# Optimization experiments

Measured on AMD Instinct MI355X. Metric: run time of the kernel, lower is better.

Reference implementation:

```python
import jax, jax.numpy as jnp
import numpy as np

NUM_HEADS = 16
QMAX = 127.0  # int8 symmetric

def fake_quant(x):
    # symmetric per-tensor int8 quantize -> dequantize (models Quantize/QLinear numerics)
    scale = jnp.maximum(jnp.max(jnp.abs(x)) / QMAX, 1e-8)
    q = jnp.clip(jnp.round(x / scale), -QMAX, QMAX) * scale
    # straight-through estimator (no-op in fwd-only, keeps fwd/bwd code identical)
    return x + jax.lax.stop_gradient(q - x)

def setup_inputs() -> dict:
    key = jax.random.key(0)
    ks = jax.random.split(key, 5)
    B, T, C = 2, 2048, 1024
    return {
        "x": jax.random.normal(ks[0], (B, T, C), jnp.float32),
        "Wqkv": jax.random.normal(ks[1], (3 * C, C), jnp.float32) * (C ** -0.5),
        "bqkv": jax.random.normal(ks[2], (3 * C,), jnp.float32) * 0.01,
        "Wproj": jax.random.normal(ks[3], (C, C), jnp.float32) * (C ** -0.5),
        "bproj": jax.random.normal(ks[4], (C,), jnp.float32) * 0.01,
    }

def reference(x, Wqkv, bqkv, Wproj, bproj):
    B, T, C = x.shape
    H = NUM_HEADS
    D = C // H
    scale = D ** -0.5
    # quantized input + quantized-weight linear (dequantized to fp32 afterwards)
    xq = fake_quant(x)
    qkv = xq @ fake_quant(Wqkv).T + bqkv                      # [B, T, 3C]
    qkv = qkv.reshape(B, T, 3, H, D).transpose(2, 0, 3, 1, 4)  # [3, B, H, T, D]
    q, k, v = qkv[0], qkv[1], qkv[2]
    scores = jnp.einsum("bhqd,bhkd->bhqk", q, k) * scale       # [B, H, T, T]
    causal = jnp.triu(jnp.full((T, T), -jnp.inf, jnp.float32), k=1)
    attn = jax.nn.softmax(scores + causal, axis=-1)
    # dropout: eval mode -> identity
    out = jnp.einsum("bhqk,bhkd->bhqd", attn, v)               # [B, H, T, D]
    out = out.transpose(0, 2, 1, 3).reshape(B, T, C)
    outq = fake_quant(out)
    return outq @ fake_quant(Wproj).T + bproj
```

## Files before the change

### kernel.cpp

```cpp
#include <hip/hip_runtime.h>
#include <hip/hip_bf16.h>
#include <stdint.h>

typedef __bf16 bf16_t;
typedef bf16_t bf16x4 __attribute__((ext_vector_type(4)));
typedef bf16_t bf16x8 __attribute__((ext_vector_type(8)));
typedef short s16x4 __attribute__((ext_vector_type(4)));
typedef int i32x4 __attribute__((ext_vector_type(4)));
typedef float f32x4 __attribute__((ext_vector_type(4)));

#define QMAXF 127.0f

__device__ __forceinline__ void gl16(const void* g, void* l) {
  __builtin_amdgcn_global_load_lds(
      (__attribute__((address_space(1))) void*)(g),
      (__attribute__((address_space(3))) void*)(l), 16, 0, 0);
}

__global__ __launch_bounds__(256) void amax3_kernel(const float* __restrict__ p0, int n0,
                                                    const float* __restrict__ p1, int n1,
                                                    const float* __restrict__ p2, int n2,
                                                    float* __restrict__ dst) {
  const float* p; int n; float* d; int b0, nb;
  if (blockIdx.x < 512)      { p = p0; n = n0; d = dst + 0; b0 = 0;   nb = 512; }
  else if (blockIdx.x < 768) { p = p1; n = n1; d = dst + 1; b0 = 512; nb = 256; }
  else                       { p = p2; n = n2; d = dst + 2; b0 = 768; nb = 128; }
  const int n4 = n >> 2;
  const int stride = nb * 256;
  float m = 0.f;
  for (int i = (blockIdx.x - b0) * 256 + threadIdx.x; i < n4; i += stride) {
    const f32x4 v = ((const f32x4*)p)[i];
    m = fmaxf(m, fmaxf(fmaxf(fabsf(v[0]), fabsf(v[1])), fmaxf(fabsf(v[2]), fabsf(v[3]))));
  }
#pragma unroll
  for (int dd = 1; dd < 64; dd <<= 1) m = fmaxf(m, __shfl_xor(m, dd));
  __shared__ float sm[4];
  if ((threadIdx.x & 63) == 0) sm[threadIdx.x >> 6] = m;
  __syncthreads();
  if (threadIdx.x == 0) {
    float mm = fmaxf(fmaxf(sm[0], sm[1]), fmaxf(sm[2], sm[3]));
    atomicMax((int*)d, __float_as_int(mm));
  }
}

__device__ __forceinline__ void quant_body(const float* __restrict__ p, int n,
                                           const float* __restrict__ amax,
                                           int8_t* __restrict__ q, int bid, int nb) {
  const float s = fmaxf(amax[0] / QMAXF, 1e-8f);
  const int n4 = n >> 2;
  const int stride = nb * 256;
  for (int i = bid * 256 + (int)threadIdx.x; i < n4; i += stride) {
    const f32x4 v = ((const f32x4*)p)[i];
    int r[4];
#pragma unroll
    for (int j = 0; j < 4; j++) {
      float t = rintf(v[j] / s);
      t = fminf(127.f, fmaxf(-127.f, t));
      r[j] = (int)t;
    }
    ((uint32_t*)q)[i] = (uint32_t)(r[0] & 0xff) | ((uint32_t)(r[1] & 0xff) << 8) |
                        ((uint32_t)(r[2] & 0xff) << 16) | ((uint32_t)(r[3] & 0xff) << 24);
  }
}

__global__ __launch_bounds__(256) void quant3_kernel(const float* __restrict__ p0, int n0,
                                                     const float* __restrict__ p1, int n1,
                                                     const float* __restrict__ p2, int n2,
                                                     const float* __restrict__ amax,
                                                     int8_t* __restrict__ q0,
                                                     int8_t* __restrict__ q1,
                                                     int8_t* __restrict__ q2) {
  if (blockIdx.x < 512)      quant_body(p0, n0, amax + 0, q0, blockIdx.x, 512);
  else if (blockIdx.x < 768) quant_body(p1, n1, amax + 1, q1, blockIdx.x - 512, 256);
  else                       quant_body(p2, n2, amax + 2, q2, blockIdx.x - 768, 128);
}

__global__ __launch_bounds__(256) void quant_kernel(const float* __restrict__ p, int n,
                                                    const float* __restrict__ amax,
                                                    int8_t* __restrict__ q) {
  quant_body(p, n, amax, q, blockIdx.x, gridDim.x);
}

template <int MODE>
__global__ __launch_bounds__(256) void gemm_i8_kernel(
    const int8_t* __restrict__ A, const int8_t* __restrict__ Bw,
    const float* __restrict__ amaxA, const float* __restrict__ amaxB,
    const float* __restrict__ bias,
    bf16_t* __restrict__ qkv_out, bf16_t* __restrict__ vt_out, float* __restrict__ f_out) {
  constexpr int K = 1024;
  __shared__ int8_t As[128 * 64];
  __shared__ int8_t Bs[128 * 64];
  const int tid = threadIdx.x;
  const int lane = tid & 63;
  const int w = tid >> 6, wr = w >> 1, wc = w & 1;
  const int l15 = lane & 15, lg = lane >> 4;
  const int bm = blockIdx.y * 128, bn = blockIdx.x * 128;

  const int sr = tid >> 2;
  const int sc = (tid & 3) * 16;
  const int8_t* gA = A + (size_t)(bm + sr) * K + sc;
  const int8_t* gB = Bw + (size_t)(bn + sr) * K + sc;
  int8_t* lA = As + tid * 16;
  int8_t* lB = Bs + tid * 16;

  i32x4 acc[4][4] = {};

  for (int k0 = 0; k0 < K; k0 += 64) {
    __syncthreads();
    gl16(gA + k0, lA);
    gl16(gA + 64 * K + k0, lA + 4096);
    gl16(gB + k0, lB);
    gl16(gB + 64 * K + k0, lB + 4096);
    __syncthreads();
    i32x4 aF[4], bF[4];
#pragma unroll
    for (int m = 0; m < 4; m++)
      aF[m] = *(const i32x4*)(As + (wr * 64 + m * 16 + l15) * 64 + lg * 16);
#pragma unroll
    for (int n = 0; n < 4; n++)
      bF[n] = *(const i32x4*)(Bs + (wc * 64 + n * 16 + l15) * 64 + lg * 16);
#pragma unroll
    for (int m = 0; m < 4; m++)
#pragma unroll
      for (int n = 0; n < 4; n++)
        acc[m][n] = __builtin_amdgcn_mfma_i32_16x16x64_i8(aF[m], bF[n], acc[m][n], 0, 0, 0);
  }

  const float sA = fmaxf(amaxA[0] / QMAXF, 1e-8f);
  const float sB = fmaxf(amaxB[0] / QMAXF, 1e-8f);
  const float s = sA * sB;

#pragma unroll
  for (int m = 0; m < 4; m++) {
#pragma unroll
    for (int n = 0; n < 4; n++) {
      const int c = bn + wc * 64 + n * 16 + l15;
      const float bs = bias[c];
      const int r0 = bm + wr * 64 + m * 16 + lg * 4;
      float vv[4];
#pragma unroll
      for (int reg = 0; reg < 4; reg++) vv[reg] = (float)acc[m][n][reg] * s + bs;
      if (MODE == 0) {
        const int which = c >> 10, hd = c & 1023;
        if (which < 2) {
#pragma unroll
          for (int reg = 0; reg < 4; reg++) {
            const int r = r0 + reg;
            const int b = r >> 11, t = r & 2047;
            qkv_out[(size_t)which * (32u * 2048 * 64) +
                    (size_t)((((b << 4) + (hd >> 6)) * 2048 + t) << 6) + (hd & 63)] = (bf16_t)vv[reg];
          }
        } else {
          const int b = r0 >> 11, t0 = r0 & 2047;
          const int h = hd >> 6, d = hd & 63;
          bf16x4 pk;
#pragma unroll
          for (int reg = 0; reg < 4; reg++) pk[reg] = (bf16_t)vv[reg];
          *(bf16x4*)(vt_out + ((size_t)((b << 4) + h) * 64 + d) * 2048 + t0) = pk;
        }
      } else {
#pragma unroll
        for (int reg = 0; reg < 4; reg++) f_out[(size_t)(r0 + reg) * 1024 + c] = vv[reg];
      }
    }
  }
}

__global__ __launch_bounds__(128) void attn_kernel(
    const bf16_t* __restrict__ Qg, const bf16_t* __restrict__ Kg, const bf16_t* __restrict__ VTg,
    float* __restrict__ Out, float* __restrict__ amax_out) {
  const int bh = blockIdx.x;
  const int pairi = blockIdx.y;
  const int tid = threadIdx.x, lane = tid & 63, w = tid >> 6;
  const int l15 = lane & 15, lg = lane >> 4;
  const int b = bh >> 4, h = bh & 15;

  const bf16_t* Qp = Qg + (size_t)bh * 2048 * 64;
  const char* Kbase = (const char*)(Kg + (size_t)bh * 2048 * 64);
  const char* Vbase = (const char*)(VTg + (size_t)bh * 64 * 2048);

  __shared__ __align__(16) bf16_t Kb[2][4096];
  __shared__ __align__(16) bf16_t Vb[2][4096];

  float am = 0.f;
  const float CSC = 0.18033688f;

  auto stage = [&](int kv0, int buf) {
#pragma unroll
    for (int i = 0; i < 8; i++) {
      const int o = i * 1024 + lane * 16;
      const int row = o >> 7;
      const int sbc = (o & 127) ^ ((row & 7) << 4);
      if (w == 0)
        gl16(Kbase + (size_t)(kv0 + row) * 128 + sbc, (char*)Kb[buf] + o);
      else
        gl16(Vbase + (size_t)row * 4096 + (size_t)kv0 * 2 + sbc, (char*)Vb[buf] + o);
    }
  };

  for (int half = 0; half < 2; ++half) {
    const int S = half ? (63 - pairi) : pairi;
    const int qb = S * 32 + w * 16;
    const int nt = (S >> 1) + 1;
    const int qrow = qb + l15;

    bf16x8 qf[2];
#pragma unroll
    for (int ks = 0; ks < 2; ks++)
      qf[ks] = *(const bf16x8*)(Qp + (size_t)(qb + l15) * 64 + ks * 32 + lg * 8);

    f32x4 acc[4] = {};
    float mrow = -1e30f, lsum = 0.f;

    stage(0, 0);
    __syncthreads();

    for (int it = 0; it < nt; ++it) {
      const int cur = it & 1;
      const int kv0 = it * 64;
      if (it + 1 < nt) stage(kv0 + 64, cur ^ 1);

      bf16x8 kF[4][2];
#pragma unroll
      for (int rf = 0; rf < 4; rf++)
#pragma unroll
        for (int ks = 0; ks < 2; ks++) {
          const int row = rf * 16 + l15;
          kF[rf][ks] = *(const bf16x8*)((const char*)Kb[cur] + row * 128 +
                                        ((ks * 64 + lg * 16) ^ ((row & 7) << 4)));
        }
      f32x4 sfT[4] = {};
      __builtin_amdgcn_s_setprio(1);
#pragma unroll
      for (int rf = 0; rf < 4; rf++)
#pragma unroll
        for (int ks = 0; ks < 2; ks++)
          sfT[rf] = __builtin_amdgcn_mfma_f32_16x16x32_bf16(kF[rf][ks], qf[ks], sfT[rf], 0, 0, 0);
      __builtin_amdgcn_s_setprio(0);

      s16x4 vB[4][4];
#pragma unroll
      for (int cf = 0; cf < 4; cf++)
#pragma unroll
        for (int rf = 0; rf < 4; rf++) {
          const int row = cf * 16 + l15;
          vB[cf][rf] = *(const s16x4*)((const char*)Vb[cur] + row * 128 +
                                       (((rf * 32 + lg * 8)) ^ ((row & 7) << 4)));
        }

      float a[16];
      const bool need_mask = (it == nt - 1);
#pragma unroll
      for (int rf = 0; rf < 4; rf++)
#pragma unroll
        for (int reg = 0; reg < 4; reg++) {
          float v = sfT[rf][reg] * CSC;
          if (need_mask && (kv0 + rf * 16 + lg * 4 + reg > qrow)) v = -1e30f;
          a[rf * 4 + reg] = v;
        }
      float mx = a[0];
#pragma unroll
      for (int i = 1; i < 16; i++) mx = fmaxf(mx, a[i]);
      mx = fmaxf(mx, __shfl_xor(mx, 16));
      mx = fmaxf(mx, __shfl_xor(mx, 32));

      if (!__all(mx <= mrow + 11.5416f)) {
        const float mnew = fmaxf(mrow, mx);
        const float alpha = __builtin_amdgcn_exp2f(mrow - mnew);
        float av[4];
#pragma unroll
        for (int reg = 0; reg < 4; reg++) av[reg] = __shfl(alpha, lg * 4 + reg);
#pragma unroll
        for (int cf = 0; cf < 4; cf++)
#pragma unroll
          for (int reg = 0; reg < 4; reg++) acc[cf][reg] *= av[reg];
        lsum *= alpha;
        mrow = mnew;
      }

      float p[16], rs = 0.f;
#pragma unroll
      for (int i = 0; i < 16; i++) { p[i] = __builtin_amdgcn_exp2f(a[i] - mrow); rs += p[i]; }
      rs += __shfl_xor(rs, 16);
      rs += __shfl_xor(rs, 32);
      lsum += rs;

      s16x4 pa[4];
#pragma unroll
      for (int rf = 0; rf < 4; rf++) {
        bf16x4 t;
#pragma unroll
        for (int reg = 0; reg < 4; reg++) t[reg] = (bf16_t)p[rf * 4 + reg];
        pa[rf] = __builtin_bit_cast(s16x4, t);
      }
      __builtin_amdgcn_s_setprio(1);
#pragma unroll
      for (int cf = 0; cf < 4; cf++)
#pragma unroll
        for (int rf = 0; rf < 4; rf++)
          acc[cf] = __builtin_amdgcn_mfma_f32_16x16x16bf16_1k(pa[rf], vB[cf][rf], acc[cf], 0, 0, 0);
      __builtin_amdgcn_s_setprio(0);

      __syncthreads();
    }

    const float inv = 1.0f / lsum;
    float iq[4];
#pragma unroll
    for (int reg = 0; reg < 4; reg++) iq[reg] = __shfl(inv, lg * 4 + reg);
#pragma unroll
    for (int cf = 0; cf < 4; cf++)
#pragma unroll
      for (int reg = 0; reg < 4; reg++) {
        const float v = acc[cf][reg] * iq[reg];
        am = fmaxf(am, fabsf(v));
        const int t = qb + lg * 4 + reg;
        Out[(size_t)(b * 2048 + t) * 1024 + h * 64 + cf * 16 + l15] = v;
      }
  }

#pragma unroll
  for (int dd = 1; dd < 64; dd <<= 1) am = fmaxf(am, __shfl_xor(am, dd));
  if (lane == 0) atomicMax((int*)amax_out, __float_as_int(am));
}

extern "C" void kernel_launch(void* const* d_in, const int* in_sizes, int n_in,
                              void* d_out, int out_size, void* d_ws, size_t ws_size,
                              hipStream_t stream) {
  const float* x = (const float*)d_in[0];
  const float* Wqkv = (const float*)d_in[1];
  const float* bqkv = (const float*)d_in[2];
  const float* Wproj = (const float*)d_in[3];
  const float* bproj = (const float*)d_in[4];
  float* out = (float*)d_out;

  char* ws = (char*)d_ws;
  float* amax = (float*)ws;
  int8_t* xq = (int8_t*)(ws + 256);
  int8_t* wqq = xq + (size_t)4096 * 1024;
  int8_t* wpq = wqq + (size_t)3072 * 1024;
  bf16_t* qkv = (bf16_t*)(ws + 8388864);
  bf16_t* Q = qkv;
  bf16_t* Kk = qkv + (size_t)32 * 2048 * 64;
  bf16_t* VT = qkv + (size_t)2 * 32 * 2048 * 64;
  float* aout = (float*)(ws + 33554688);
  int8_t* outq = (int8_t*)(ws + 50331904);

  hipMemsetAsync(amax, 0, 16, stream);
  amax3_kernel<<<896, 256, 0, stream>>>(x, 4194304, Wqkv, 3145728, Wproj, 1048576, amax);
  quant3_kernel<<<896, 256, 0, stream>>>(x, 4194304, Wqkv, 3145728, Wproj, 1048576, amax,
                                         xq, wqq, wpq);
  gemm_i8_kernel<0><<<dim3(24, 32), 256, 0, stream>>>(xq, wqq, amax + 0, amax + 1, bqkv,
                                                      qkv, VT, nullptr);
  attn_kernel<<<dim3(32, 32), 128, 0, stream>>>(Q, Kk, VT, aout, amax + 3);
  quant_kernel<<<512, 256, 0, stream>>>(aout, 4194304, amax + 3, outq);
  gemm_i8_kernel<1><<<dim3(8, 32), 256, 0, stream>>>(outq, wpq, amax + 3, amax + 2, bproj,
                                                     nullptr, nullptr, out);
}
```

Baseline: 144.4 us.

## Split attention into one query tile per block, single-buffer V, fold scale into Q

Attention blocks now each handle one 32-row query tile, launched heaviest-first over a 64-wide grid, instead of pairing a light and a heavy tile in one block. V staging becomes single-buffered, with a mid-iteration barrier so the next V tile loads after the current one has been read into registers. This halves V shared memory, which may raise occupancy. The softmax scale constant is multiplied into Q in the QKV GEMM epilogue, removing a per-score multiply. In exchange the kernel launches more blocks, adds a second barrier per iteration, and stores Q with an extra bf16 rounding after the scaling.

```diff
diff --git a/kernel.cpp b/kernel.cpp
--- a/kernel.cpp
+++ b/kernel.cpp
@@ -10,6 +10,7 @@
 typedef float f32x4 __attribute__((ext_vector_type(4)));
 
 #define QMAXF 127.0f
+#define CSC 0.18033688f
 
 __device__ __forceinline__ void gl16(const void* g, void* l) {
   __builtin_amdgcn_global_load_lds(
@@ -143,12 +144,14 @@
       if (MODE == 0) {
         const int which = c >> 10, hd = c & 1023;
         if (which < 2) {
+          const float qs = (which == 0) ? CSC : 1.0f;
 #pragma unroll
           for (int reg = 0; reg < 4; reg++) {
             const int r = r0 + reg;
             const int b = r >> 11, t = r & 2047;
             qkv_out[(size_t)which * (32u * 2048 * 64) +
-                    (size_t)((((b << 4) + (hd >> 6)) * 2048 + t) << 6) + (hd & 63)] = (bf16_t)vv[reg];
+                    (size_t)((((b << 4) + (hd >> 6)) * 2048 + t) << 6) + (hd & 63)] =
+                (bf16_t)(vv[reg] * qs);
           }
         } else {
           const int b = r0 >> 11, t0 = r0 & 2047;
@@ -170,7 +173,7 @@
     const bf16_t* __restrict__ Qg, const bf16_t* __restrict__ Kg, const bf16_t* __restrict__ VTg,
     float* __restrict__ Out, float* __restrict__ amax_out) {
   const int bh = blockIdx.x;
-  const int pairi = blockIdx.y;
+  const int S = 63 - (int)blockIdx.y;
   const int tid = threadIdx.x, lane = tid & 63, w = tid >> 6;
   const int l15 = lane & 15, lg = lane >> 4;
   const int b = bh >> 4, h = bh & 15;
@@ -180,144 +183,157 @@
   const char* Vbase = (const char*)(VTg + (size_t)bh * 64 * 2048);
 
   __shared__ __align__(16) bf16_t Kb[2][4096];
-  __shared__ __align__(16) bf16_t Vb[2][4096];
-
+  __shared__ __align__(16) bf16_t Vb[4096];
+
+  auto stageK = [&](int kv0, int buf) {
+    if (w == 0) {
+#pragma unroll
+      for (int i = 0; i < 8; i++) {
+        const int o = i * 1024 + lane * 16;
+        const int row = o >> 7;
+        const int sbc = (o & 127) ^ ((row & 7) << 4);
+        gl16(Kbase + (size_t)(kv0 + row) * 128 + sbc, (char*)Kb[buf] + o);
+      }
+    }
+  };
+  auto stageV = [&](int kv0) {
+    if (w == 1) {
+#pragma unroll
+      for (int i = 0; i < 8; i++) {
+        const int o = i * 1024 + lane * 16;
+        const int row = o >> 7;
+        const int sbc = (o & 127) ^ ((row & 7) << 4);
+        gl16(Vbase + (size_t)row * 4096 + (size_t)kv0 * 2 + sbc, (char*)Vb + o);
+      }
+    }
+  };
+
+  const int qb = S * 32 + w * 16;
+  const int nt = (S >> 1) + 1;
+  const int qrow = qb + l15;
+
+  bf16x8 qf[2];
+#pragma unroll
+  for (int ks = 0; ks < 2; ks++)
+    qf[ks] = *(const bf16x8*)(Qp + (size_t)(qb + l15) * 64 + ks * 32 + lg * 8);
+
+  f32x4 acc[4] = {};
+  float mrow = -1e30f, lsum = 0.f;
+
+  stageK(0, 0);
+  stageV(0);
+  __syncthreads();
+
+  for (int it = 0; it < nt; ++it) {
+    const int cur = it & 1;
+    const int kv0 = it * 64;
+    if (it + 1 < nt) stageK(kv0 + 64, cur ^ 1);
+
+    bf16x8 kF[4][2];
+#pragma unroll
+    for (int rf = 0; rf < 4; rf++)
+#pragma unroll
+      for (int ks = 0; ks < 2; ks++) {
+        const int row = rf * 16 + l15;
+        kF[rf][ks] = *(const bf16x8*)((const char*)Kb[cur] + row * 128 +
+                                      ((ks * 64 + lg * 16) ^ ((row & 7) << 4)));
+      }
+    f32x4 sfT[4] = {};
+    __builtin_amdgcn_s_setprio(1);
+#pragma unroll
+    for (int rf = 0; rf < 4; rf++)
+#pragma unroll
+      for (int ks = 0; ks < 2; ks++)
+        sfT[rf] = __builtin_amdgcn_mfma_f32_16x16x32_bf16(kF[rf][ks], qf[ks], sfT[rf], 0, 0, 0);
+    __builtin_amdgcn_s_setprio(0);
+
+    s16x4 vB[4][4];
+#pragma unroll
+    for (int cf = 0; cf < 4; cf++)
+#pragma unroll
+      for (int rf = 0; rf < 4; rf++) {
+        const int row = cf * 16 + l15;
+        vB[cf][rf] = *(const s16x4*)((const char*)Vb + row * 128 +
+                                     ((rf * 32 + lg * 8) ^ ((row & 7) << 4)));
+      }
+    asm volatile("s_waitcnt lgkmcnt(0)" ::: "memory");
+    __builtin_amdgcn_sched_barrier(0);
+    __builtin_amdgcn_s_barrier();
+    __builtin_amdgcn_sched_barrier(0);
+    if (it + 1 < nt) stageV(kv0 + 64);
+
+    float a[16];
+    const bool need_mask = (it == nt - 1);
+#pragma unroll
+    for (int rf = 0; rf < 4; rf++)
+#pragma unroll
+      for (int reg = 0; reg < 4; reg++) {
+        float v = sfT[rf][reg];
+        if (need_mask && (kv0 + rf * 16 + lg * 4 + reg > qrow)) v = -1e30f;
+        a[rf * 4 + reg] = v;
+      }
+    float mx = a[0];
+#pragma unroll
+    for (int i = 1; i < 16; i++) mx = fmaxf(mx, a[i]);
+    mx = fmaxf(mx, __shfl_xor(mx, 16));
+    mx = fmaxf(mx, __shfl_xor(mx, 32));
+
+    if (!__all(mx <= mrow + 11.5416f)) {
+      const float mnew = fmaxf(mrow, mx);
+      const float alpha = __builtin_amdgcn_exp2f(mrow - mnew);
+      float av[4];
+#pragma unroll
+      for (int reg = 0; reg < 4; reg++) av[reg] = __shfl(alpha, lg * 4 + reg);
+#pragma unroll
+      for (int cf = 0; cf < 4; cf++)
+#pragma unroll
+        for (int reg = 0; reg < 4; reg++) acc[cf][reg] *= av[reg];
+      lsum *= alpha;
+      mrow = mnew;
+    }
+
+    float p[16], rs = 0.f;
+#pragma unroll
+    for (int i = 0; i < 16; i++) { p[i] = __builtin_amdgcn_exp2f(a[i] - mrow); rs += p[i]; }
+    rs += __shfl_xor(rs, 16);
+    rs += __shfl_xor(rs, 32);
+    lsum += rs;
+
+    s16x4 pa[4];
+#pragma unroll
+    for (int rf = 0; rf < 4; rf++) {
+      bf16x4 t;
+#pragma unroll
+      for (int reg = 0; reg < 4; reg++) t[reg] = (bf16_t)p[rf * 4 + reg];
+      pa[rf] = __builtin_bit_cast(s16x4, t);
+    }
+    __builtin_amdgcn_s_setprio(1);
+#pragma unroll
+    for (int cf = 0; cf < 4; cf++)
+#pragma unroll
+      for (int rf = 0; rf < 4; rf++)
+        acc[cf] = __builtin_amdgcn_mfma_f32_16x16x16bf16_1k(pa[rf], vB[cf][rf], acc[cf], 0, 0, 0);
+    __builtin_amdgcn_s_setprio(0);
+
+    asm volatile("s_waitcnt vmcnt(0)" ::: "memory");
+    __builtin_amdgcn_sched_barrier(0);
+    __builtin_amdgcn_s_barrier();
+  }
+
+  const float inv = 1.0f / lsum;
+  float iq[4];
+#pragma unroll
+  for (int reg = 0; reg < 4; reg++) iq[reg] = __shfl(inv, lg * 4 + reg);
   float am = 0.f;
-  const float CSC = 0.18033688f;
-
-  auto stage = [&](int kv0, int buf) {
-#pragma unroll
-    for (int i = 0; i < 8; i++) {
-      const int o = i * 1024 + lane * 16;
-      const int row = o >> 7;
-      const int sbc = (o & 127) ^ ((row & 7) << 4);
-      if (w == 0)
-        gl16(Kbase + (size_t)(kv0 + row) * 128 + sbc, (char*)Kb[buf] + o);
-      else
-        gl16(Vbase + (size_t)row * 4096 + (size_t)kv0 * 2 + sbc, (char*)Vb[buf] + o);
-    }
-  };
-
-  for (int half = 0; half < 2; ++half) {
-    const int S = half ? (63 - pairi) : pairi;
-    const int qb = S * 32 + w * 16;
-    const int nt = (S >> 1) + 1;
-    const int qrow = qb + l15;
-
-    bf16x8 qf[2];
-#pragma unroll
-    for (int ks = 0; ks < 2; ks++)
-      qf[ks] = *(const bf16x8*)(Qp + (size_t)(qb + l15) * 64 + ks * 32 + lg * 8);
-
-    f32x4 acc[4] = {};
-    float mrow = -1e30f, lsum = 0.f;
-
-    stage(0, 0);
-    __syncthreads();
-
-    for (int it = 0; it < nt; ++it) {
-      const int cur = it & 1;
-      const int kv0 = it * 64;
-      if (it + 1 < nt) stage(kv0 + 64, cur ^ 1);
-
-      bf16x8 kF[4][2];
-#pragma unroll
-      for (int rf = 0; rf < 4; rf++)
-#pragma unroll
-        for (int ks = 0; ks < 2; ks++) {
-          const int row = rf * 16 + l15;
-          kF[rf][ks] = *(const bf16x8*)((const char*)Kb[cur] + row * 128 +
-                                        ((ks * 64 + lg * 16) ^ ((row & 7) << 4)));
-        }
-      f32x4 sfT[4] = {};
-      __builtin_amdgcn_s_setprio(1);
-#pragma unroll
-      for (int rf = 0; rf < 4; rf++)
-#pragma unroll
-        for (int ks = 0; ks < 2; ks++)
-          sfT[rf] = __builtin_amdgcn_mfma_f32_16x16x32_bf16(kF[rf][ks], qf[ks], sfT[rf], 0, 0, 0);
-      __builtin_amdgcn_s_setprio(0);
-
-      s16x4 vB[4][4];
-#pragma unroll
-      for (int cf = 0; cf < 4; cf++)
-#pragma unroll
-        for (int rf = 0; rf < 4; rf++) {
-          const int row = cf * 16 + l15;
-          vB[cf][rf] = *(const s16x4*)((const char*)Vb[cur] + row * 128 +
-                                       (((rf * 32 + lg * 8)) ^ ((row & 7) << 4)));
-        }
-
-      float a[16];
-      const bool need_mask = (it == nt - 1);
-#pragma unroll
-      for (int rf = 0; rf < 4; rf++)
-#pragma unroll
-        for (int reg = 0; reg < 4; reg++) {
-          float v = sfT[rf][reg] * CSC;
-          if (need_mask && (kv0 + rf * 16 + lg * 4 + reg > qrow)) v = -1e30f;
-          a[rf * 4 + reg] = v;
-        }
-      float mx = a[0];
-#pragma unroll
-      for (int i = 1; i < 16; i++) mx = fmaxf(mx, a[i]);
-      mx = fmaxf(mx, __shfl_xor(mx, 16));
-      mx = fmaxf(mx, __shfl_xor(mx, 32));
-
-      if (!__all(mx <= mrow + 11.5416f)) {
-        const float mnew = fmaxf(mrow, mx);
-        const float alpha = __builtin_amdgcn_exp2f(mrow - mnew);
-        float av[4];
-#pragma unroll
-        for (int reg = 0; reg < 4; reg++) av[reg] = __shfl(alpha, lg * 4 + reg);
-#pragma unroll
-        for (int cf = 0; cf < 4; cf++)
-#pragma unroll
-          for (int reg = 0; reg < 4; reg++) acc[cf][reg] *= av[reg];
-        lsum *= alpha;
-        mrow = mnew;
-      }
-
-      float p[16], rs = 0.f;
-#pragma unroll
-      for (int i = 0; i < 16; i++) { p[i] = __builtin_amdgcn_exp2f(a[i] - mrow); rs += p[i]; }
-      rs += __shfl_xor(rs, 16);
-      rs += __shfl_xor(rs, 32);
-      lsum += rs;
-
-      s16x4 pa[4];
-#pragma unroll
-      for (int rf = 0; rf < 4; rf++) {
-        bf16x4 t;
-#pragma unroll
-        for (int reg = 0; reg < 4; reg++) t[reg] = (bf16_t)p[rf * 4 + reg];
-        pa[rf] = __builtin_bit_cast(s16x4, t);
-      }
-      __builtin_amdgcn_s_setprio(1);
-#pragma unroll
-      for (int cf = 0; cf < 4; cf++)
-#pragma unroll
-        for (int rf = 0; rf < 4; rf++)
-          acc[cf] = __builtin_amdgcn_mfma_f32_16x16x16bf16_1k(pa[rf], vB[cf][rf], acc[cf], 0, 0, 0);
-      __builtin_amdgcn_s_setprio(0);
-
-      __syncthreads();
-    }
-
-    const float inv = 1.0f / lsum;
-    float iq[4];
-#pragma unroll
-    for (int reg = 0; reg < 4; reg++) iq[reg] = __shfl(inv, lg * 4 + reg);
-#pragma unroll
-    for (int cf = 0; cf < 4; cf++)
-#pragma unroll
-      for (int reg = 0; reg < 4; reg++) {
-        const float v = acc[cf][reg] * iq[reg];
-        am = fmaxf(am, fabsf(v));
-        const int t = qb + lg * 4 + reg;
-        Out[(size_t)(b * 2048 + t) * 1024 + h * 64 + cf * 16 + l15] = v;
-      }
-  }
+#pragma unroll
+  for (int cf = 0; cf < 4; cf++)
+#pragma unroll
+    for (int reg = 0; reg < 4; reg++) {
+      const float v = acc[cf][reg] * iq[reg];
+      am = fmaxf(am, fabsf(v));
+      const int t = qb + lg * 4 + reg;
+      Out[(size_t)(b * 2048 + t) * 1024 + h * 64 + cf * 16 + l15] = v;
+    }
 
 #pragma unroll
   for (int dd = 1; dd < 64; dd <<= 1) am = fmaxf(am, __shfl_xor(am, dd));
@@ -352,7 +368,7 @@
                                          xq, wqq, wpq);
   gemm_i8_kernel<0><<<dim3(24, 32), 256, 0, stream>>>(xq, wqq, amax + 0, amax + 1, bqkv,
                                                       qkv, VT, nullptr);
-  attn_kernel<<<dim3(32, 32), 128, 0, stream>>>(Q, Kk, VT, aout, amax + 3);
+  attn_kernel<<<dim3(32, 64), 128, 0, stream>>>(Q, Kk, VT, aout, amax + 3);
   quant_kernel<<<512, 256, 0, stream>>>(aout, 4194304, amax + 3, outq);
   gemm_i8_kernel<1><<<dim3(8, 32), 256, 0, stream>>>(outq, wpq, amax + 3, amax + 2, bproj,
                                                      nullptr, nullptr, out);
```

After: 153.6 us. +6.4%, slower.
